# Kernel tuning notes

Hardware: AMD Instinct MI355X
Metric: run time of the kernel (lower is better)

## Reference

```python
import jax, jax.numpy as jnp
import numpy as np

NEG = -1e6  # mask fill value used by d2l.sequence_mask


def setup_inputs() -> dict:
    key = jax.random.key(0)
    k1, k2, k3, k4, k5, k6, k7 = jax.random.split(key, 7)
    B, Q, K, DQ, DK, H, DV = 8, 256, 1024, 256, 256, 128, 128
    queries = jax.random.normal(k1, (B, Q, DQ), dtype=jnp.float32)
    keys = jax.random.normal(k2, (B, K, DK), dtype=jnp.float32)
    values = jax.random.normal(k3, (B, K, DV), dtype=jnp.float32)
    valid_lens = jax.random.randint(k4, (B,), 1, K + 1, dtype=jnp.int32)
    # learned params (nn.Linear stores weight as [out, in]; apply as x @ W.T)
    W_q = jax.random.normal(k5, (H, DQ), dtype=jnp.float32) / np.sqrt(DQ)
    W_k = jax.random.normal(k6, (H, DK), dtype=jnp.float32) / np.sqrt(DK)
    w_v = jax.random.normal(k7, (H,), dtype=jnp.float32) / np.sqrt(H)
    return {"queries": queries, "keys": keys, "values": values,
            "valid_lens": valid_lens, "W_q": W_q, "W_k": W_k, "w_v": w_v}


def reference(queries, keys, values, valid_lens, W_q, W_k, w_v):
    # projections
    q = jnp.einsum('bqd,hd->bqh', queries, W_q)   # [B,Q,H]
    k = jnp.einsum('bkd,hd->bkh', keys, W_k)      # [B,K,H]
    # broadcast add + tanh -> [B,Q,K,H] (the fusion-headroom intermediate)
    features = jnp.tanh(q[:, :, None, :] + k[:, None, :, :])
    scores = jnp.einsum('bqkh,h->bqk', features, w_v)  # [B,Q,K]
    # masked softmax: valid_lens is per-batch (dim==1 path)
    klen = scores.shape[-1]
    mask = jnp.arange(klen)[None, None, :] < valid_lens[:, None, None]
    scores = jnp.where(mask, scores, NEG)
    weights = jax.nn.softmax(scores, axis=-1)
    # dropout is identity in eval mode
    return jnp.einsum('bqk,bkv->bqv', weights, values)
```

## Files before the change

### kernel.cpp

```cpp
#include <hip/hip_runtime.h>


#define Bb 8
#define Qn 256
#define Kk 1024
#define Dd 256
#define Hh 128
#define DVv 128

__device__ __forceinline__ float fexp2(float x) { return __builtin_amdgcn_exp2f(x); }
__device__ __forceinline__ float frcp(float x)  { return __builtin_amdgcn_rcpf(x); }

__global__ __launch_bounds__(256)
void repack_w(const float* __restrict__ Wq, const float* __restrict__ Wk,
              float4* __restrict__ Wq4T, float4* __restrict__ Wk4T)
{
    const int blk = blockIdx.x;
    const float* src = (blk < 32) ? Wq : Wk;
    float4*      dst = (blk < 32) ? Wq4T : Wk4T;
    const int idx = (blk & 31) * 256 + threadIdx.x;
    const int g = idx >> 7;
    const int h = idx & 127;
    dst[idx] = *(const float4*)(src + (size_t)h * Dd + g * 4);
}

__global__ __launch_bounds__(512)
void proj_exp_kernel(const float* __restrict__ queries,
                     const float* __restrict__ keys,
                     const float4* __restrict__ Wq4T,
                     const float4* __restrict__ Wk4T,
                     float* __restrict__ EqT,
                     float* __restrict__ EkT)
{
    __shared__ __align__(16) float Xs[16 * 256];
    const int blk = blockIdx.x;
    const float* X; const float4* W4; float* outT; int RB; int i0;
    if (blk < 128) { X = queries; W4 = Wq4T; outT = EqT; RB = Qn; i0 = blk * 16; }
    else           { X = keys;    W4 = Wk4T; outT = EkT; RB = Kk; i0 = (blk - 128) * 16; }
    const int tid = threadIdx.x;
    const int h   = tid & 127;
    const int r4  = __builtin_amdgcn_readfirstlane(tid >> 7);

    {
        const float4* xsrc = (const float4*)(X + (size_t)i0 * Dd);
#pragma unroll
        for (int s = 0; s < 2; ++s) {
            const int idx = tid + 512 * s;
            *(float4*)(Xs + idx * 4) = xsrc[idx];
        }
    }
    __syncthreads();

    float acc[4] = {0.f, 0.f, 0.f, 0.f};
    const float4* wp = W4 + h;
    const float*  xr = Xs + (r4 * 4) * 256;
#pragma unroll 8
    for (int g = 0; g < 64; ++g) {
        const float4 w = wp[(size_t)g * 128];
#pragma unroll
        for (int i = 0; i < 4; ++i) {
            const float4 x = *(const float4*)(xr + i * 256 + g * 4);
            acc[i] = fmaf(x.x, w.x, acc[i]);
            acc[i] = fmaf(x.y, w.y, acc[i]);
            acc[i] = fmaf(x.z, w.z, acc[i]);
            acc[i] = fmaf(x.w, w.w, acc[i]);
        }
    }
    const int b    = i0 / RB;
    const int rloc = (i0 % RB) + r4 * 4;
    float4 o;
    o.x = fexp2(acc[0] * 2.885390082f);
    o.y = fexp2(acc[1] * 2.885390082f);
    o.z = fexp2(acc[2] * 2.885390082f);
    o.w = fexp2(acc[3] * 2.885390082f);
    *(float4*)(outT + (size_t)b * Hh * RB + (size_t)h * RB + rloc) = o;
}

#define SCORE4(q4, w4, ea, eb, ec, ed, accref)                                \
    {                                                                          \
        const float A_ = fmaf((q4).x, (ea), 1.f), B_ = fmaf((q4).y, (eb), 1.f);\
        const float C_ = fmaf((q4).z, (ec), 1.f), E_ = fmaf((q4).w, (ed), 1.f);\
        const float AB_ = A_ * B_, CE_ = C_ * E_;                              \
        const float N_ = fmaf(fmaf((w4).x, B_, (w4).y * A_), CE_,              \
                              fmaf((w4).z, E_, (w4).w * C_) * AB_);            \
        (accref) = fmaf(N_, frcp(AB_ * CE_), (accref));                        \
    }

__global__ __launch_bounds__(1024, 4)
void score_softmax_pv_kernel(const float* __restrict__ EqT,
                             const float* __restrict__ EkT,
                             const float* __restrict__ wv,
                             const int* __restrict__ valid_lens,
                             const float* __restrict__ values,
                             float* __restrict__ out)
{
    __shared__ __align__(16) float  s_sc[4][Kk];
    __shared__ __align__(16) float  eqsT[4][Hh];
    __shared__ __align__(16) float  w2s[Hh];
    __shared__ __align__(16) float4 s_part[15][4][32];
    __shared__ float s_qmax[4][4];
    __shared__ float s_qsum[4][4];

    const int blk  = blockIdx.x;
    const int qt   = blk >> 3;
    const int b    = (blk & 7) ^ ((qt & 32) ? 4 : 0);
    const int q0   = qt * 4;
    const int len  = valid_lens[b];
    const int tid  = threadIdx.x;
    const int lane = tid & 63;
    const int wave = __builtin_amdgcn_readfirstlane(tid >> 6);

    if (tid < 128) {
        const float4 v = *(const float4*)(EqT + (size_t)b * Hh * Qn + (size_t)tid * Qn + q0);
        eqsT[0][tid] = v.x; eqsT[1][tid] = v.y; eqsT[2][tid] = v.z; eqsT[3][tid] = v.w;
    } else if (tid < 256) {
        w2s[tid - 128] = -2.0f * wv[tid - 128];
    }
    __syncthreads();

    const int qh = __builtin_amdgcn_readfirstlane(tid >> 9);
    const int kg = tid & 511;
    const int kspan = ((tid >> 6) & 7) << 7;

    if (kspan < len) {
        const float2* ek2 = (const float2*)(EkT + (size_t)b * Hh * Kk) + kg;
        const int qA = (qh << 1);
        float acc[2][2] = {};
#pragma unroll 2
        for (int hg = 0; hg < 32; ++hg) {
            const int h = hg << 2;
            const float2 e0 = ek2[(size_t)(h + 0) * (Kk / 2)];
            const float2 e1 = ek2[(size_t)(h + 1) * (Kk / 2)];
            const float2 e2 = ek2[(size_t)(h + 2) * (Kk / 2)];
            const float2 e3 = ek2[(size_t)(h + 3) * (Kk / 2)];
            const float4 w4 = *(const float4*)(w2s + h);
#pragma unroll
            for (int qi = 0; qi < 2; ++qi) {
                const float4 q4 = *(const float4*)(&eqsT[qA + qi][h]);
                SCORE4(q4, w4, e0.x, e1.x, e2.x, e3.x, acc[qi][0]);
                SCORE4(q4, w4, e0.y, e1.y, e2.y, e3.y, acc[qi][1]);
            }
        }
#pragma unroll
        for (int qi = 0; qi < 2; ++qi)
            *(float2*)(&s_sc[qA + qi][kg << 1]) = make_float2(acc[qi][0], acc[qi][1]);
    }
    __syncthreads();

    {
        const int q    = wave & 3;
        const int qtr  = wave >> 2;
        const int base = qtr * 256;
        const int hi   = (base + 256 < len) ? base + 256 : len;
        float m = -3.0e38f;
        for (int i = base + lane; i < hi; i += 64) m = fmaxf(m, s_sc[q][i]);
#pragma unroll
        for (int off = 32; off > 0; off >>= 1) m = fmaxf(m, __shfl_xor(m, off));
        if (lane == 0) s_qmax[q][qtr] = m;
        __syncthreads();
        const float gm = fmaxf(fmaxf(s_qmax[q][0], s_qmax[q][1]),
                               fmaxf(s_qmax[q][2], s_qmax[q][3]));
        float sum = 0.f;
        for (int i = base + lane; i < hi; i += 64) {
            const float p = fexp2((s_sc[q][i] - gm) * 1.44269504f);
            s_sc[q][i] = p;
            sum += p;
        }
#pragma unroll
        for (int off = 32; off > 0; off >>= 1) sum += __shfl_xor(sum, off);
        if (lane == 0) s_qsum[q][qtr] = sum;
    }
    __syncthreads();

    {
        const int slice = tid >> 5;
        const int l32   = tid & 31;
        const int v4    = l32 << 2;
        const float* vp = values + (size_t)b * Kk * DVv + v4;
        float a[4][4];
#pragma unroll
        for (int q = 0; q < 4; ++q) { a[q][0]=0.f; a[q][1]=0.f; a[q][2]=0.f; a[q][3]=0.f; }
        for (int k = slice; k < len; k += 32) {
            const float4 val = *(const float4*)(vp + (size_t)k * DVv);
            const float w0 = s_sc[0][k], w1 = s_sc[1][k], w2 = s_sc[2][k], w3 = s_sc[3][k];
            a[0][0] = fmaf(w0, val.x, a[0][0]);
            a[0][1] = fmaf(w0, val.y, a[0][1]);
            a[0][2] = fmaf(w0, val.z, a[0][2]);
            a[0][3] = fmaf(w0, val.w, a[0][3]);
            a[1][0] = fmaf(w1, val.x, a[1][0]);
            a[1][1] = fmaf(w1, val.y, a[1][1]);
            a[1][2] = fmaf(w1, val.z, a[1][2]);
            a[1][3] = fmaf(w1, val.w, a[1][3]);
            a[2][0] = fmaf(w2, val.x, a[2][0]);
            a[2][1] = fmaf(w2, val.y, a[2][1]);
            a[2][2] = fmaf(w2, val.z, a[2][2]);
            a[2][3] = fmaf(w2, val.w, a[2][3]);
            a[3][0] = fmaf(w3, val.x, a[3][0]);
            a[3][1] = fmaf(w3, val.y, a[3][1]);
            a[3][2] = fmaf(w3, val.z, a[3][2]);
            a[3][3] = fmaf(w3, val.w, a[3][3]);
        }
#pragma unroll
        for (int q = 0; q < 4; ++q)
#pragma unroll
            for (int x = 0; x < 4; ++x) a[q][x] += __shfl_xor(a[q][x], 32);
        if (wave > 0 && lane < 32) {
#pragma unroll
            for (int q = 0; q < 4; ++q)
                s_part[wave - 1][q][l32] = make_float4(a[q][0], a[q][1], a[q][2], a[q][3]);
        }
        __syncthreads();
        if (wave == 0 && lane < 32) {
#pragma unroll
            for (int q = 0; q < 4; ++q) {
                float r0 = a[q][0], r1 = a[q][1], r2 = a[q][2], r3 = a[q][3];
#pragma unroll
                for (int w = 0; w < 15; ++w) {
                    const float4 p = s_part[w][q][l32];
                    r0 += p.x; r1 += p.y; r2 += p.z; r3 += p.w;
                }
                const float inv = frcp(s_qsum[q][0] + s_qsum[q][1] +
                                       s_qsum[q][2] + s_qsum[q][3]);
                *(float4*)(out + (size_t)(b * Qn + q0 + q) * DVv + v4) =
                    make_float4(r0 * inv, r1 * inv, r2 * inv, r3 * inv);
            }
        }
    }
}

extern "C" void kernel_launch(void* const* d_in, const int* in_sizes, int n_in,
                              void* d_out, int out_size, void* d_ws, size_t ws_size,
                              hipStream_t stream) {
    (void)in_sizes; (void)n_in; (void)out_size; (void)ws_size;
    const float* queries    = (const float*)d_in[0];
    const float* keys       = (const float*)d_in[1];
    const float* values     = (const float*)d_in[2];
    const int*   valid_lens = (const int*)  d_in[3];
    const float* Wq         = (const float*)d_in[4];
    const float* Wk         = (const float*)d_in[5];
    const float* wvv        = (const float*)d_in[6];
    float* out = (float*)d_out;

    float* Wq4T = (float*)d_ws;
    float* Wk4T = Wq4T + (size_t)Dd * Hh;
    float* EqT  = Wk4T + (size_t)Dd * Hh;
    float* EkT  = EqT + (size_t)Bb * Hh * Qn;

    repack_w       <<<  64, 256, 0, stream>>>(Wq, Wk, (float4*)Wq4T, (float4*)Wk4T);
    proj_exp_kernel<<< 640, 512, 0, stream>>>(queries, keys, (const float4*)Wq4T,
                                              (const float4*)Wk4T, EqT, EkT);
    score_softmax_pv_kernel<<<512, 1024, 0, stream>>>(EqT, EkT, wvv, valid_lens,
                                                      values, out);
}
```

Before: 133.3 us.

## Process eight queries per block with one key per thread for more reuse

Each block now handles 8 query rows instead of 4, halving the grid to 256 blocks. In the score phase each thread takes one key column and accumulates all 8 queries, so every loaded Ek value is reused across twice as many queries, and the values rows in the PV phase are reused across 8 queries. The softmax is split into two halves per query instead of quarters. In exchange, shared memory and register pressure roughly double and the grid has only 256 blocks, which can leave compute units underused. The masked-key skip now works at 64-key granularity.

```diff
diff --git a/kernel.cpp b/kernel.cpp
--- a/kernel.cpp
+++ b/kernel.cpp
@@ -94,72 +94,69 @@
                              const float* __restrict__ values,
                              float* __restrict__ out)
 {
-    __shared__ __align__(16) float  s_sc[4][Kk];
-    __shared__ __align__(16) float  eqsT[4][Hh];
+    __shared__ __align__(16) float  s_sc[8][Kk];
+    __shared__ __align__(16) float  eqsT[8][Hh];
     __shared__ __align__(16) float  w2s[Hh];
-    __shared__ __align__(16) float4 s_part[15][4][32];
-    __shared__ float s_qmax[4][4];
-    __shared__ float s_qsum[4][4];
+    __shared__ __align__(16) float4 s_part[15][8][32];
+    __shared__ float s_qmax[8][2];
+    __shared__ float s_qsum[8][2];
 
     const int blk  = blockIdx.x;
+    const int b    = blk & 7;
     const int qt   = blk >> 3;
-    const int b    = (blk & 7) ^ ((qt & 32) ? 4 : 0);
-    const int q0   = qt * 4;
+    const int q0   = qt * 8;
     const int len  = valid_lens[b];
     const int tid  = threadIdx.x;
     const int lane = tid & 63;
     const int wave = __builtin_amdgcn_readfirstlane(tid >> 6);
 
     if (tid < 128) {
-        const float4 v = *(const float4*)(EqT + (size_t)b * Hh * Qn + (size_t)tid * Qn + q0);
-        eqsT[0][tid] = v.x; eqsT[1][tid] = v.y; eqsT[2][tid] = v.z; eqsT[3][tid] = v.w;
+        const float4 v0 = *(const float4*)(EqT + (size_t)b * Hh * Qn + (size_t)tid * Qn + q0);
+        const float4 v1 = *(const float4*)(EqT + (size_t)b * Hh * Qn + (size_t)tid * Qn + q0 + 4);
+        eqsT[0][tid] = v0.x; eqsT[1][tid] = v0.y; eqsT[2][tid] = v0.z; eqsT[3][tid] = v0.w;
+        eqsT[4][tid] = v1.x; eqsT[5][tid] = v1.y; eqsT[6][tid] = v1.z; eqsT[7][tid] = v1.w;
     } else if (tid < 256) {
         w2s[tid - 128] = -2.0f * wv[tid - 128];
     }
     __syncthreads();
 
-    const int qh = __builtin_amdgcn_readfirstlane(tid >> 9);
-    const int kg = tid & 511;
-    const int kspan = ((tid >> 6) & 7) << 7;
-
-    if (kspan < len) {
-        const float2* ek2 = (const float2*)(EkT + (size_t)b * Hh * Kk) + kg;
-        const int qA = (qh << 1);
-        float acc[2][2] = {};
+    {
+        const int kspan = (tid >> 6) << 6;
+        if (kspan < len) {
+            const float* ekp = EkT + (size_t)b * Hh * Kk + tid;
+            float acc[8] = {};
 #pragma unroll 2
-        for (int hg = 0; hg < 32; ++hg) {
-            const int h = hg << 2;
-            const float2 e0 = ek2[(size_t)(h + 0) * (Kk / 2)];
-            const float2 e1 = ek2[(size_t)(h + 1) * (Kk / 2)];
-            const float2 e2 = ek2[(size_t)(h + 2) * (Kk / 2)];
-            const float2 e3 = ek2[(size_t)(h + 3) * (Kk / 2)];
-            const float4 w4 = *(const float4*)(w2s + h);
-#pragma unroll
-            for (int qi = 0; qi < 2; ++qi) {
-                const float4 q4 = *(const float4*)(&eqsT[qA + qi][h]);
-                SCORE4(q4, w4, e0.x, e1.x, e2.x, e3.x, acc[qi][0]);
-                SCORE4(q4, w4, e0.y, e1.y, e2.y, e3.y, acc[qi][1]);
+            for (int hg = 0; hg < 32; ++hg) {
+                const int h = hg << 2;
+                const float e0 = ekp[(size_t)(h + 0) * Kk];
+                const float e1 = ekp[(size_t)(h + 1) * Kk];
+                const float e2 = ekp[(size_t)(h + 2) * Kk];
+                const float e3 = ekp[(size_t)(h + 3) * Kk];
+                const float4 w4 = *(const float4*)(w2s + h);
+#pragma unroll
+                for (int q = 0; q < 8; ++q) {
+                    const float4 q4 = *(const float4*)(&eqsT[q][h]);
+                    SCORE4(q4, w4, e0, e1, e2, e3, acc[q]);
+                }
             }
-        }
-#pragma unroll
-        for (int qi = 0; qi < 2; ++qi)
-            *(float2*)(&s_sc[qA + qi][kg << 1]) = make_float2(acc[qi][0], acc[qi][1]);
-    }
-    __syncthreads();
-
-    {
-        const int q    = wave & 3;
-        const int qtr  = wave >> 2;
-        const int base = qtr * 256;
-        const int hi   = (base + 256 < len) ? base + 256 : len;
+#pragma unroll
+            for (int q = 0; q < 8; ++q) s_sc[q][tid] = acc[q];
+        }
+    }
+    __syncthreads();
+
+    {
+        const int q    = wave & 7;
+        const int half = wave >> 3;
+        const int base = half * 512;
+        const int hi   = (base + 512 < len) ? base + 512 : len;
         float m = -3.0e38f;
         for (int i = base + lane; i < hi; i += 64) m = fmaxf(m, s_sc[q][i]);
 #pragma unroll
         for (int off = 32; off > 0; off >>= 1) m = fmaxf(m, __shfl_xor(m, off));
-        if (lane == 0) s_qmax[q][qtr] = m;
+        if (lane == 0) s_qmax[q][half] = m;
         __syncthreads();
-        const float gm = fmaxf(fmaxf(s_qmax[q][0], s_qmax[q][1]),
-                               fmaxf(s_qmax[q][2], s_qmax[q][3]));
+        const float gm = fmaxf(s_qmax[q][0], s_qmax[q][1]);
         float sum = 0.f;
         for (int i = base + lane; i < hi; i += 64) {
             const float p = fexp2((s_sc[q][i] - gm) * 1.44269504f);
@@ -168,7 +165,7 @@
         }
 #pragma unroll
         for (int off = 32; off > 0; off >>= 1) sum += __shfl_xor(sum, off);
-        if (lane == 0) s_qsum[q][qtr] = sum;
+        if (lane == 0) s_qsum[q][half] = sum;
     }
     __syncthreads();
 
@@ -177,50 +174,40 @@
         const int l32   = tid & 31;
         const int v4    = l32 << 2;
         const float* vp = values + (size_t)b * Kk * DVv + v4;
-        float a[4][4];
-#pragma unroll
-        for (int q = 0; q < 4; ++q) { a[q][0]=0.f; a[q][1]=0.f; a[q][2]=0.f; a[q][3]=0.f; }
+        float a[8][4];
+#pragma unroll
+        for (int q = 0; q < 8; ++q) { a[q][0]=0.f; a[q][1]=0.f; a[q][2]=0.f; a[q][3]=0.f; }
         for (int k = slice; k < len; k += 32) {
             const float4 val = *(const float4*)(vp + (size_t)k * DVv);
-            const float w0 = s_sc[0][k], w1 = s_sc[1][k], w2 = s_sc[2][k], w3 = s_sc[3][k];
-            a[0][0] = fmaf(w0, val.x, a[0][0]);
-            a[0][1] = fmaf(w0, val.y, a[0][1]);
-            a[0][2] = fmaf(w0, val.z, a[0][2]);
-            a[0][3] = fmaf(w0, val.w, a[0][3]);
-            a[1][0] = fmaf(w1, val.x, a[1][0]);
-            a[1][1] = fmaf(w1, val.y, a[1][1]);
-            a[1][2] = fmaf(w1, val.z, a[1][2]);
-            a[1][3] = fmaf(w1, val.w, a[1][3]);
-            a[2][0] = fmaf(w2, val.x, a[2][0]);
-            a[2][1] = fmaf(w2, val.y, a[2][1]);
-            a[2][2] = fmaf(w2, val.z, a[2][2]);
-            a[2][3] = fmaf(w2, val.w, a[2][3]);
-            a[3][0] = fmaf(w3, val.x, a[3][0]);
-            a[3][1] = fmaf(w3, val.y, a[3][1]);
-            a[3][2] = fmaf(w3, val.z, a[3][2]);
-            a[3][3] = fmaf(w3, val.w, a[3][3]);
-        }
-#pragma unroll
-        for (int q = 0; q < 4; ++q)
+#pragma unroll
+            for (int q = 0; q < 8; ++q) {
+                const float w = s_sc[q][k];
+                a[q][0] = fmaf(w, val.x, a[q][0]);
+                a[q][1] = fmaf(w, val.y, a[q][1]);
+                a[q][2] = fmaf(w, val.z, a[q][2]);
+                a[q][3] = fmaf(w, val.w, a[q][3]);
+            }
+        }
+#pragma unroll
+        for (int q = 0; q < 8; ++q)
 #pragma unroll
             for (int x = 0; x < 4; ++x) a[q][x] += __shfl_xor(a[q][x], 32);
         if (wave > 0 && lane < 32) {
 #pragma unroll
-            for (int q = 0; q < 4; ++q)
+            for (int q = 0; q < 8; ++q)
                 s_part[wave - 1][q][l32] = make_float4(a[q][0], a[q][1], a[q][2], a[q][3]);
         }
         __syncthreads();
         if (wave == 0 && lane < 32) {
 #pragma unroll
-            for (int q = 0; q < 4; ++q) {
+            for (int q = 0; q < 8; ++q) {
                 float r0 = a[q][0], r1 = a[q][1], r2 = a[q][2], r3 = a[q][3];
 #pragma unroll
                 for (int w = 0; w < 15; ++w) {
                     const float4 p = s_part[w][q][l32];
                     r0 += p.x; r1 += p.y; r2 += p.z; r3 += p.w;
                 }
-                const float inv = frcp(s_qsum[q][0] + s_qsum[q][1] +
-                                       s_qsum[q][2] + s_qsum[q][3]);
+                const float inv = frcp(s_qsum[q][0] + s_qsum[q][1]);
                 *(float4*)(out + (size_t)(b * Qn + q0 + q) * DVv + v4) =
                     make_float4(r0 * inv, r1 * inv, r2 * inv, r3 * inv);
             }
@@ -249,6 +236,6 @@
     repack_w       <<<  64, 256, 0, stream>>>(Wq, Wk, (float4*)Wq4T, (float4*)Wk4T);
     proj_exp_kernel<<< 640, 512, 0, stream>>>(queries, keys, (const float4*)Wq4T,
                                               (const float4*)Wk4T, EqT, EkT);
-    score_softmax_pv_kernel<<<512, 1024, 0, stream>>>(EqT, EkT, wvv, valid_lens,
+    score_softmax_pv_kernel<<<256, 1024, 0, stream>>>(EqT, EkT, wvv, valid_lens,
                                                       values, out);
 }
```

After: 136.9 us. 2.7% more time.
